# Kernel optimization log

Measured on AMD Instinct MI355X. Metric: run time of the kernel, lower is better.

## Reference

```python
import jax, jax.numpy as jnp
import numpy as np

B, F, D = 2048, 40, 32
CIN = (64, 64)


def _glorot(key, shape):
    fan_in, fan_out = shape[1] * shape[2], shape[0] * shape[2]
    std = jnp.sqrt(2.0 / (fan_in + fan_out)).astype(jnp.float32)
    return jax.random.normal(key, shape, dtype=jnp.float32) * std


def setup_inputs() -> dict:
    key = jax.random.key(0)
    kx, k0, k1 = jax.random.split(key, 3)
    x = jax.random.normal(kx, (B, F, D), dtype=jnp.float32)
    W0 = _glorot(k0, (CIN[0], F * F, D))
    b0 = jnp.zeros((CIN[0],), dtype=jnp.float32)
    W1 = _glorot(k1, (CIN[1], F * CIN[0], D))
    b1 = jnp.zeros((CIN[1],), dtype=jnp.float32)
    return {"x": x, "W0": W0, "b0": b0, "W1": W1, "b1": b1}


def _cin_step(x0, xk, W, b):
    # x0: (B,F,D)  xk: (B,H,D)  W: (O, H*F, D)  b: (O,)
    Bn, H, Dn = xk.shape
    Fn = x0.shape[1]
    # outer product per embedding channel, h-major flatten as in tf.reshape
    z = jnp.einsum('bhd,bfd->bhfd', xk, x0).reshape(Bn, H * Fn, Dn)
    # per-embedding-channel contraction against weights: (B,D,O)
    y = jnp.einsum('bhd,ohd->bdo', z, W) + b
    y = jax.nn.relu(y)
    return jnp.transpose(y, (0, 2, 1))  # (B,O,D)


def reference(x, W0, b0, W1, b1):
    x1 = _cin_step(x, x, W0, b0)
    x2 = _cin_step(x, x1, W1, b1)
    final = jnp.concatenate([x, x1, x2], axis=1)  # (B, F+O0+O1, D)
    return jnp.sum(final, axis=-1)  # (B, F+O0+O1)
```

## Files before the change

### kernel.cpp

```cpp
#include <hip/hip_runtime.h>

typedef unsigned int   u32;
typedef unsigned short u16;
typedef _Float16       f16;

using f16x8  = __attribute__((ext_vector_type(8)))  _Float16;
using f32x16 = __attribute__((ext_vector_type(16))) float;

#define LLDS16(G, L) __builtin_amdgcn_global_load_lds( \
  (const __attribute__((address_space(1))) u32*)(G), \
  (__attribute__((address_space(3))) u32*)(L), 16, 0, 0)

#define WAITV(N) { asm volatile("s_waitcnt vmcnt(" #N ")" ::: "memory"); \
                   __builtin_amdgcn_sched_barrier(0); }
#define FENCE_BAR() { asm volatile("s_waitcnt lgkmcnt(0)" ::: "memory"); \
                      __builtin_amdgcn_sched_barrier(0); \
                      __builtin_amdgcn_s_barrier(); \
                      __builtin_amdgcn_sched_barrier(0); }
#define BAR() { __builtin_amdgcn_s_barrier(); __builtin_amdgcn_sched_barrier(0); }
#define KEEP(x) asm volatile("" : "+v"(x))

__global__ __launch_bounds__(256)
void xprep(const float* __restrict__ in, f16* __restrict__ out,
           float* __restrict__ osum){
  __shared__ float tile[32][33];
  const int tid = threadIdx.x;
  const int r0  = blockIdx.x << 5;
  const int c   = tid & 31;
  const int rp  = tid >> 5;
#pragma unroll
  for (int p = 0; p < 4; ++p){
    const int r = (p << 3) + rp;
    float v = in[(size_t)(r0 + r) * 32 + c];
    tile[r][c] = v;
    float s = v;
#pragma unroll
    for (int off = 16; off > 0; off >>= 1) s += __shfl_xor(s, off, 32);
    if (c == 0){
      const int row = r0 + r;
      osum[(size_t)(row / 40) * 168 + (row % 40)] = s;
    }
  }
  __syncthreads();
#pragma unroll
  for (int p = 0; p < 4; ++p){
    const int dd = (p << 3) + rp;
    out[(size_t)dd * 81920 + r0 + c] = (f16)tile[c][dd];
  }
}

__global__ __launch_bounds__(256)
void wprep(const float* __restrict__ W0, const float* __restrict__ W1,
           f16* __restrict__ out0, f16* __restrict__ out1){
  __shared__ u16 t[32 * 530];
  int kb = blockIdx.x;
  const float* in; f16* out; int K;
  if (kb < 200){ in = W0; out = out0; K = 1600; }
  else         { kb -= 200; in = W1; out = out1; K = 2560; }
  const int tid = threadIdx.x;
  const int kbase = kb << 3;
#pragma unroll 4
  for (int i = 0; i < 64; ++i){
    const int idx = tid + (i << 8);
    const int o   = idx >> 8;
    const int rem = idx & 255;
    const int e   = rem >> 5;
    const int dd  = rem & 31;
    const float v = in[(size_t)o * (K * 32) + (size_t)(kbase + e) * 32 + dd];
    union { f16 h; u16 u; } cv; cv.h = (f16)v;
    t[dd * 530 + o * 8 + e] = cv.u;
  }
  __syncthreads();
  const u32* t32 = (const u32*)t;
  u32* o32 = (u32*)out;
  const int obase = kb << 8;
#pragma unroll 4
  for (int i = 0; i < 32; ++i){
    const int idx = tid + (i << 8);
    const int dd  = idx >> 8;
    const int rem = idx & 255;
    o32[(size_t)dd * (K * 32) + obase + rem] = t32[dd * 265 + rem];
  }
}

template<int H>
__global__ __launch_bounds__(512, 2)
void cin_gemm(const f16* __restrict__ xt,
              const f16* __restrict__ xkt,
              const f16* __restrict__ Wp,
              const float* __restrict__ bias,
              f16*       __restrict__ yt)
{
  constexpr int K     = H * 40;
  constexpr int NT    = K / 320;
  constexpr int X0OFF = 81920;
  constexpr int XKOFF = 110592;
  constexpr int X0MS  = 32 * 112;
  constexpr int XHMS  = (H == 64) ? 32 * 144 : 32 * 112;
  constexpr int SMEM  = (H == 64) ? 147456 : 110592;

  const int bid = blockIdx.x;
  const int d   = ((bid & 7) << 2) | ((bid >> 3) & 3);
  const int b0  = (bid >> 5) << 8;
  const int tid = threadIdx.x;
  const int wv  = tid >> 6;
  const int wr  = wv >> 1;
  const int wc  = wv & 1;
  const int l   = tid & 63;
  const int hi  = l >> 5;
  const int lr  = l & 31;

  __shared__ char smem[SMEM];

  const f16* gW = Wp + (size_t)d * (K * 64);

#define ISSUE_TILE(T, BUF) do { \
    const f16* gt = gW + (size_t)(T) * 20480 + wv * 2560 + l * 8; \
    char* lb = smem + (BUF) * 40960 + wv * 5120; \
    _Pragma("unroll") \
    for (int i = 0; i < 5; ++i) LLDS16(gt + i * 512, lb + i * 1024); \
  } while (0)

  ISSUE_TILE(0, 0);
  ISSUE_TILE(1, 1);

  {
    const uint4* src = (const uint4*)(xt + (size_t)d * 81920 + (size_t)b0 * 40);
#pragma unroll
    for (int it = 0; it < 3; ++it){
      const int idx = tid + (it << 9);
      if (idx < 1280){
        const int r = idx / 5, c = idx - r * 5;
        *(uint4*)(smem + X0OFF + r * 112 + c * 16) = src[idx];
      }
    }
  }
  if constexpr (H == 64){
    const uint4* src = (const uint4*)(xkt + (size_t)d * 131072 + (size_t)b0 * 64);
#pragma unroll
    for (int it = 0; it < 4; ++it){
      const int idx = tid + (it << 9);
      const int r = idx >> 3, c = idx & 7;
      *(uint4*)(smem + XKOFF + r * 144 + c * 16) = src[idx];
    }
  }
  __syncthreads();

  const char* x0row = smem + X0OFF + (wr * 64 + lr) * 112;
  const char* xhrow = (H == 64) ? (smem + XKOFF + (wr * 64 + lr) * 144) : x0row;

  f16x8 sl[2][5];
#pragma unroll
  for (int m = 0; m < 2; ++m){
    const char* xe = x0row + m * X0MS + hi * 16;
#pragma unroll
    for (int t = 0; t < 4; ++t) sl[m][t] = *(const f16x8*)(xe + t * 16);
    sl[m][4] = *(const f16x8*)(x0row + m * X0MS + (hi ? 0 : 64));
  }
  KEEP(sl[0][0]); KEEP(sl[0][1]); KEEP(sl[0][2]); KEEP(sl[0][3]); KEEP(sl[0][4]);
  KEEP(sl[1][0]); KEEP(sl[1][1]); KEEP(sl[1][2]); KEEP(sl[1][3]); KEEP(sl[1][4]);

  f16x8 xh0 = *(const f16x8*)(xhrow);
  f16x8 xh1 = *(const f16x8*)(xhrow + XHMS);

  f32x16 acc0 = {0,0,0,0,0,0,0,0,0,0,0,0,0,0,0,0};
  f32x16 acc1 = {0,0,0,0,0,0,0,0,0,0,0,0,0,0,0,0};

  const int vb = hi * 1024 + wc * 512 + lr * 16;

  static constexpr int J0[10]  = {0,4,3,2,1,0,4,3,2,1};
  static constexpr int H0[10]  = {0,0,1,2,3,4,4,5,6,7};
  static constexpr int H0b[10] = {0,1,1,2,3,4,5,5,6,7};
  static constexpr int S0[10]  = {0,1,0,0,0,0,1,0,0,0};
  static constexpr int J2[10]  = {2,1,0,4,3,2,1,0,4,3};
  static constexpr int H2[10]  = {0,1,2,2,3,4,5,6,6,7};
  static constexpr int H2b[10] = {0,1,2,3,3,4,5,6,7,7};
  static constexpr int S2[10]  = {0,0,0,1,0,0,0,0,1,0};

  for (int t = 0; t < NT; ++t){
    const char* bb = smem + (t & 1) * 40960 + vb;
    const f16x8 xhn0 = *(const f16x8*)(xhrow + (t + 1) * 16);
    const f16x8 xhn1 = *(const f16x8*)(xhrow + XHMS + (t + 1) * 16);
#pragma unroll
    for (int si = 0; si < 10; ++si){
      const f16x8 bf0 = *(const f16x8*)(bb + (si * 4) * 1024);
      const f16x8 bf2 = *(const f16x8*)(bb + (si * 4 + 2) * 1024);
      const f16 xa00 = (S0[si] && hi) ? xh0[H0b[si]] : xh0[H0[si]];
      const f16 xa01 = (S0[si] && hi) ? xh1[H0b[si]] : xh1[H0[si]];
      const f16 xa20 = (S2[si] && hi) ? xh0[H2b[si]] : xh0[H2[si]];
      const f16 xa21 = (S2[si] && hi) ? xh1[H2b[si]] : xh1[H2[si]];
      acc0 = __builtin_amdgcn_mfma_f32_32x32x16_f16(sl[0][J0[si]] * xa00, bf0, acc0, 0, 0, 0);
      acc1 = __builtin_amdgcn_mfma_f32_32x32x16_f16(sl[1][J0[si]] * xa01, bf0, acc1, 0, 0, 0);
      acc0 = __builtin_amdgcn_mfma_f32_32x32x16_f16(sl[0][J2[si]] * xa20, bf2, acc0, 0, 0, 0);
      acc1 = __builtin_amdgcn_mfma_f32_32x32x16_f16(sl[1][J2[si]] * xa21, bf2, acc1, 0, 0, 0);
    }
    FENCE_BAR();
    if (t + 2 < NT){
      ISSUE_TILE(t + 2, t & 1);
      WAITV(5);
    } else {
      WAITV(0);
    }
    BAR();
    xh0 = xhn0; xh1 = xhn1;
  }

  const float bv = bias[(wc << 5) + lr];
  u16* yw = (u16*)(smem + wv * 4608);
#pragma unroll
  for (int m = 0; m < 2; ++m)
#pragma unroll
    for (int reg = 0; reg < 16; ++reg){
      const int row = (m << 5) + (reg & 3) + ((reg >> 2) << 3) + (hi << 2);
      float v = (m ? acc1[reg] : acc0[reg]) + bv;
      v = v > 0.f ? v : 0.f;
      union { f16 h; u16 u; } cv; cv.h = (f16)v;
      yw[row * 36 + lr] = cv.u;
    }
  asm volatile("s_waitcnt lgkmcnt(0)" ::: "memory");
  {
    f16* ydst = yt + (size_t)d * 131072;
#pragma unroll
    for (int j = 0; j < 4; ++j){
      const int row = (j << 4) + (l >> 2);
      const int ch  = l & 3;
      const f16x8 vv = *(const f16x8*)((const char*)yw + row * 72 + ch * 16);
      *(f16x8*)(ydst + (size_t)(b0 + (wr << 6) + row) * 64 + (wc << 5) + (ch << 3)) = vv;
    }
  }
#undef ISSUE_TILE
}

__global__ __launch_bounds__(128)
void finalize(const f16* __restrict__ x1t, const f16* __restrict__ y2t,
              float* __restrict__ out){
  const int b = blockIdx.x;
  const int t = threadIdx.x;
  if (t < 64){
    float s = 0.f;
#pragma unroll
    for (int d = 0; d < 32; ++d) s += (float)x1t[(size_t)d * 131072 + (size_t)b * 64 + t];
    out[(size_t)b * 168 + 40 + t] = s;
  } else {
    const int o = t - 64;
    float s = 0.f;
#pragma unroll
    for (int d = 0; d < 32; ++d) s += (float)y2t[(size_t)d * 131072 + (size_t)b * 64 + o];
    out[(size_t)b * 168 + 104 + o] = s;
  }
}

extern "C" void kernel_launch(void* const* d_in, const int* in_sizes, int n_in,
                              void* d_out, int out_size, void* d_ws, size_t ws_size,
                              hipStream_t stream){
  const float* x   = (const float*)d_in[0];
  const float* W0  = (const float*)d_in[1];
  const float* b0v = (const float*)d_in[2];
  const float* W1  = (const float*)d_in[3];
  const float* b1v = (const float*)d_in[4];
  float* out = (float*)d_out;

  char* ws = (char*)d_ws;
  f16* xt  = (f16*)(ws + 0);
  f16* W0p = (f16*)(ws + 5242880);
  f16* W1p = (f16*)(ws + 11796480);
  f16* x1t = (f16*)(ws + 22282240);
  f16* y2t = (f16*)(ws + 30670848);

  xprep<<<2560, 256, 0, stream>>>(x, xt, out);
  wprep<<<520, 256, 0, stream>>>(W0, W1, W0p, W1p);

  cin_gemm<40><<<256, 512, 0, stream>>>(xt, nullptr, W0p, b0v, x1t);
  cin_gemm<64><<<256, 512, 0, stream>>>(xt, x1t,     W1p, b1v, y2t);

  finalize<<<2048, 128, 0, stream>>>(x1t, y2t, out);
}
```

Before: 62.75 us.

## Fuse both CIN layers into one kernel with atomic row-sum epilogue

```diff
diff --git a/kernel.cpp b/kernel.cpp
--- a/kernel.cpp
+++ b/kernel.cpp
@@ -21,83 +21,78 @@
 #define KEEP(x) asm volatile("" : "+v"(x))
 
 __global__ __launch_bounds__(256)
-void xprep(const float* __restrict__ in, f16* __restrict__ out,
-           float* __restrict__ osum){
-  __shared__ float tile[32][33];
+void prep(const float* __restrict__ x,
+          const float* __restrict__ W0, const float* __restrict__ W1,
+          f16* __restrict__ xt, f16* __restrict__ W0p, f16* __restrict__ W1p,
+          float* __restrict__ out){
+  __shared__ char shm[33920];
   const int tid = threadIdx.x;
-  const int r0  = blockIdx.x << 5;
-  const int c   = tid & 31;
-  const int rp  = tid >> 5;
-#pragma unroll
-  for (int p = 0; p < 4; ++p){
-    const int r = (p << 3) + rp;
-    float v = in[(size_t)(r0 + r) * 32 + c];
-    tile[r][c] = v;
-    float s = v;
-#pragma unroll
-    for (int off = 16; off > 0; off >>= 1) s += __shfl_xor(s, off, 32);
-    if (c == 0){
-      const int row = r0 + r;
-      osum[(size_t)(row / 40) * 168 + (row % 40)] = s;
-    }
-  }
-  __syncthreads();
-#pragma unroll
-  for (int p = 0; p < 4; ++p){
-    const int dd = (p << 3) + rp;
-    out[(size_t)dd * 81920 + r0 + c] = (f16)tile[c][dd];
+  if (blockIdx.x < 2560){
+    float (*tile)[33] = (float(*)[33])shm;
+    const int r0 = blockIdx.x << 5;
+    const int c  = tid & 31;
+    const int rp = tid >> 5;
+#pragma unroll
+    for (int p = 0; p < 4; ++p){
+      const int r = (p << 3) + rp;
+      float v = x[(size_t)(r0 + r) * 32 + c];
+      tile[r][c] = v;
+      float s = v;
+#pragma unroll
+      for (int off = 16; off > 0; off >>= 1) s += __shfl_xor(s, off, 32);
+      if (c == 0){
+        const int row = r0 + r;
+        out[(size_t)(row / 40) * 168 + (row % 40)] = s;
+      }
+    }
+    __syncthreads();
+#pragma unroll
+    for (int p = 0; p < 4; ++p){
+      const int dd = (p << 3) + rp;
+      xt[(size_t)dd * 81920 + r0 + c] = (f16)tile[c][dd];
+    }
+  } else {
+    u16* t = (u16*)shm;
+    int kb = blockIdx.x - 2560;
+    const float* in; f16* outp; int K;
+    if (kb < 200){ in = W0; outp = W0p; K = 1600; }
+    else         { kb -= 200; in = W1; outp = W1p; K = 2560; }
+    const int kbase = kb << 3;
+#pragma unroll 4
+    for (int i = 0; i < 64; ++i){
+      const int idx = tid + (i << 8);
+      const int o   = idx >> 8;
+      const int rem = idx & 255;
+      const int e   = rem >> 5;
+      const int dd  = rem & 31;
+      const float v = in[(size_t)o * (K * 32) + (size_t)(kbase + e) * 32 + dd];
+      union { f16 h; u16 u; } cv; cv.h = (f16)v;
+      t[dd * 530 + o * 8 + e] = cv.u;
+    }
+    __syncthreads();
+    const u32* t32 = (const u32*)t;
+    u32* o32 = (u32*)outp;
+    const int obase = kb << 8;
+#pragma unroll 4
+    for (int i = 0; i < 32; ++i){
+      const int idx = tid + (i << 8);
+      const int dd  = idx >> 8;
+      const int rem = idx & 255;
+      o32[(size_t)dd * (K * 32) + obase + rem] = t32[dd * 265 + rem];
+    }
   }
 }
 
-__global__ __launch_bounds__(256)
-void wprep(const float* __restrict__ W0, const float* __restrict__ W1,
-           f16* __restrict__ out0, f16* __restrict__ out1){
-  __shared__ u16 t[32 * 530];
-  int kb = blockIdx.x;
-  const float* in; f16* out; int K;
-  if (kb < 200){ in = W0; out = out0; K = 1600; }
-  else         { kb -= 200; in = W1; out = out1; K = 2560; }
-  const int tid = threadIdx.x;
-  const int kbase = kb << 3;
-#pragma unroll 4
-  for (int i = 0; i < 64; ++i){
-    const int idx = tid + (i << 8);
-    const int o   = idx >> 8;
-    const int rem = idx & 255;
-    const int e   = rem >> 5;
-    const int dd  = rem & 31;
-    const float v = in[(size_t)o * (K * 32) + (size_t)(kbase + e) * 32 + dd];
-    union { f16 h; u16 u; } cv; cv.h = (f16)v;
-    t[dd * 530 + o * 8 + e] = cv.u;
-  }
-  __syncthreads();
-  const u32* t32 = (const u32*)t;
-  u32* o32 = (u32*)out;
-  const int obase = kb << 8;
-#pragma unroll 4
-  for (int i = 0; i < 32; ++i){
-    const int idx = tid + (i << 8);
-    const int dd  = idx >> 8;
-    const int rem = idx & 255;
-    o32[(size_t)dd * (K * 32) + obase + rem] = t32[dd * 265 + rem];
-  }
-}
-
-template<int H>
-__global__ __launch_bounds__(512, 2)
-void cin_gemm(const f16* __restrict__ xt,
-              const f16* __restrict__ xkt,
-              const f16* __restrict__ Wp,
-              const float* __restrict__ bias,
-              f16*       __restrict__ yt)
-{
-  constexpr int K     = H * 40;
-  constexpr int NT    = K / 320;
+__global__ __launch_bounds__(512, 1)
+void cin_fused(const f16* __restrict__ xt,
+               const f16* __restrict__ W0p,
+               const f16* __restrict__ W1p,
+               const float* __restrict__ b0v, const float* __restrict__ b1v,
+               float* __restrict__ out){
   constexpr int X0OFF = 81920;
-  constexpr int XKOFF = 110592;
+  constexpr int X1OFF = 110592;
   constexpr int X0MS  = 32 * 112;
-  constexpr int XHMS  = (H == 64) ? 32 * 144 : 32 * 112;
-  constexpr int SMEM  = (H == 64) ? 147456 : 110592;
+  constexpr int X1MS  = 32 * 144;
 
   const int bid = blockIdx.x;
   const int d   = ((bid & 7) << 2) | ((bid >> 3) & 3);
@@ -110,19 +105,22 @@
   const int hi  = l >> 5;
   const int lr  = l & 31;
 
-  __shared__ char smem[SMEM];
-
-  const f16* gW = Wp + (size_t)d * (K * 64);
-
-#define ISSUE_TILE(T, BUF) do { \
-    const f16* gt = gW + (size_t)(T) * 20480 + wv * 2560 + l * 8; \
-    char* lb = smem + (BUF) * 40960 + wv * 5120; \
+  __shared__ char smem[147456];
+
+  const f16* gW0 = W0p + (size_t)d * 102400;
+  const f16* gW1 = W1p + (size_t)d * 163840;
+
+#define ISSUE(I) do { \
+    const f16* src_ = ((I) < 5) ? (gW0 + (size_t)(I) * 20480) \
+                                : (gW1 + (size_t)((I) - 5) * 20480); \
+    const f16* gt_ = src_ + wv * 2560 + l * 8; \
+    char* lb_ = smem + ((I) & 1) * 40960 + wv * 5120; \
     _Pragma("unroll") \
-    for (int i = 0; i < 5; ++i) LLDS16(gt + i * 512, lb + i * 1024); \
+    for (int j_ = 0; j_ < 5; ++j_) LLDS16(gt_ + j_ * 512, lb_ + j_ * 1024); \
   } while (0)
 
-  ISSUE_TILE(0, 0);
-  ISSUE_TILE(1, 1);
+  ISSUE(0);
+  ISSUE(1);
 
   {
     const uint4* src = (const uint4*)(xt + (size_t)d * 81920 + (size_t)b0 * 40);
@@ -135,19 +133,13 @@
       }
     }
   }
-  if constexpr (H == 64){
-    const uint4* src = (const uint4*)(xkt + (size_t)d * 131072 + (size_t)b0 * 64);
-#pragma unroll
-    for (int it = 0; it < 4; ++it){
-      const int idx = tid + (it << 9);
-      const int r = idx >> 3, c = idx & 7;
-      *(uint4*)(smem + XKOFF + r * 144 + c * 16) = src[idx];
-    }
-  }
   __syncthreads();
 
   const char* x0row = smem + X0OFF + (wr * 64 + lr) * 112;
-  const char* xhrow = (H == 64) ? (smem + XKOFF + (wr * 64 + lr) * 144) : x0row;
+  const char* x1row = smem + X1OFF + (wr * 64 + lr) * 144;
+  const int   hcol  = (wc << 5) + lr;
+  const float bv1   = b0v[hcol];
+  const float bv2   = b1v[hcol];
 
   f16x8 sl[2][5];
 #pragma unroll
@@ -159,9 +151,6 @@
   }
   KEEP(sl[0][0]); KEEP(sl[0][1]); KEEP(sl[0][2]); KEEP(sl[0][3]); KEEP(sl[0][4]);
   KEEP(sl[1][0]); KEEP(sl[1][1]); KEEP(sl[1][2]); KEEP(sl[1][3]); KEEP(sl[1][4]);
-
-  f16x8 xh0 = *(const f16x8*)(xhrow);
-  f16x8 xh1 = *(const f16x8*)(xhrow + XHMS);
 
   f32x16 acc0 = {0,0,0,0,0,0,0,0,0,0,0,0,0,0,0,0};
   f32x16 acc1 = {0,0,0,0,0,0,0,0,0,0,0,0,0,0,0,0};
@@ -177,77 +166,90 @@
   static constexpr int H2b[10] = {0,1,2,3,3,4,5,6,7,7};
   static constexpr int S2[10]  = {0,0,0,1,0,0,0,0,1,0};
 
-  for (int t = 0; t < NT; ++t){
-    const char* bb = smem + (t & 1) * 40960 + vb;
-    const f16x8 xhn0 = *(const f16x8*)(xhrow + (t + 1) * 16);
-    const f16x8 xhn1 = *(const f16x8*)(xhrow + XHMS + (t + 1) * 16);
-#pragma unroll
-    for (int si = 0; si < 10; ++si){
-      const f16x8 bf0 = *(const f16x8*)(bb + (si * 4) * 1024);
-      const f16x8 bf2 = *(const f16x8*)(bb + (si * 4 + 2) * 1024);
-      const f16 xa00 = (S0[si] && hi) ? xh0[H0b[si]] : xh0[H0[si]];
-      const f16 xa01 = (S0[si] && hi) ? xh1[H0b[si]] : xh1[H0[si]];
-      const f16 xa20 = (S2[si] && hi) ? xh0[H2b[si]] : xh0[H2[si]];
-      const f16 xa21 = (S2[si] && hi) ? xh1[H2b[si]] : xh1[H2[si]];
-      acc0 = __builtin_amdgcn_mfma_f32_32x32x16_f16(sl[0][J0[si]] * xa00, bf0, acc0, 0, 0, 0);
-      acc1 = __builtin_amdgcn_mfma_f32_32x32x16_f16(sl[1][J0[si]] * xa01, bf0, acc1, 0, 0, 0);
-      acc0 = __builtin_amdgcn_mfma_f32_32x32x16_f16(sl[0][J2[si]] * xa20, bf2, acc0, 0, 0, 0);
-      acc1 = __builtin_amdgcn_mfma_f32_32x32x16_f16(sl[1][J2[si]] * xa21, bf2, acc1, 0, 0, 0);
-    }
-    FENCE_BAR();
-    if (t + 2 < NT){
-      ISSUE_TILE(t + 2, t & 1);
+#define COMP(BB) do { \
+  _Pragma("unroll") \
+  for (int si = 0; si < 10; ++si){ \
+    const f16x8 bf0 = *(const f16x8*)((BB) + (si * 4) * 1024); \
+    const f16x8 bf2 = *(const f16x8*)((BB) + (si * 4 + 2) * 1024); \
+    const f16 xa00 = (S0[si] && hi) ? xh0[H0b[si]] : xh0[H0[si]]; \
+    const f16 xa01 = (S0[si] && hi) ? xh1[H0b[si]] : xh1[H0[si]]; \
+    const f16 xa20 = (S2[si] && hi) ? xh0[H2b[si]] : xh0[H2[si]]; \
+    const f16 xa21 = (S2[si] && hi) ? xh1[H2b[si]] : xh1[H2[si]]; \
+    acc0 = __builtin_amdgcn_mfma_f32_32x32x16_f16(sl[0][J0[si]] * xa00, bf0, acc0, 0, 0, 0); \
+    acc1 = __builtin_amdgcn_mfma_f32_32x32x16_f16(sl[1][J0[si]] * xa01, bf0, acc1, 0, 0, 0); \
+    acc0 = __builtin_amdgcn_mfma_f32_32x32x16_f16(sl[0][J2[si]] * xa20, bf2, acc0, 0, 0, 0); \
+    acc1 = __builtin_amdgcn_mfma_f32_32x32x16_f16(sl[1][J2[si]] * xa21, bf2, acc1, 0, 0, 0); \
+  } \
+} while (0)
+
+  {
+    f16x8 xh0 = *(const f16x8*)(x0row);
+    f16x8 xh1 = *(const f16x8*)(x0row + X0MS);
+    for (int t = 0; t < 5; ++t){
+      const char* bb = smem + (t & 1) * 40960 + vb;
+      const f16x8 xhn0 = *(const f16x8*)(x0row + (t + 1) * 16);
+      const f16x8 xhn1 = *(const f16x8*)(x0row + X0MS + (t + 1) * 16);
+      COMP(bb);
+      FENCE_BAR();
+      ISSUE(t + 2);
       WAITV(5);
-    } else {
-      WAITV(0);
-    }
+      BAR();
+      xh0 = xhn0; xh1 = xhn1;
+    }
+  }
+
+  {
+    u16* x1w = (u16*)(smem + X1OFF);
+#pragma unroll
+    for (int m = 0; m < 2; ++m)
+#pragma unroll
+      for (int reg = 0; reg < 16; ++reg){
+        const int row = (wr << 6) + (m << 5) + (reg & 3) + ((reg >> 2) << 3) + (hi << 2);
+        float v = (m ? acc1[reg] : acc0[reg]) + bv1;
+        v = v > 0.f ? v : 0.f;
+        union { f16 h; u16 u; } cv; cv.h = (f16)v;
+        x1w[row * 72 + hcol] = cv.u;
+        atomicAdd(&out[(size_t)(b0 + row) * 168 + 40 + hcol], v);
+      }
+    const f32x16 fz = {0,0,0,0,0,0,0,0,0,0,0,0,0,0,0,0};
+    acc0 = fz; acc1 = fz;
+    asm volatile("s_waitcnt lgkmcnt(0)" ::: "memory");
+    __builtin_amdgcn_sched_barrier(0);
+    WAITV(0);
     BAR();
-    xh0 = xhn0; xh1 = xhn1;
-  }
-
-  const float bv = bias[(wc << 5) + lr];
-  u16* yw = (u16*)(smem + wv * 4608);
+  }
+
+  {
+    f16x8 xh0 = *(const f16x8*)(x1row);
+    f16x8 xh1 = *(const f16x8*)(x1row + X1MS);
+    for (int t = 0; t < 8; ++t){
+      const char* bb = smem + ((t + 1) & 1) * 40960 + vb;
+      const f16x8 xhn0 = *(const f16x8*)(x1row + (t + 1) * 16);
+      const f16x8 xhn1 = *(const f16x8*)(x1row + X1MS + (t + 1) * 16);
+      COMP(bb);
+      FENCE_BAR();
+      if (t + 2 < 8){
+        ISSUE(5 + t + 2);
+        WAITV(5);
+      } else {
+        WAITV(0);
+      }
+      BAR();
+      xh0 = xhn0; xh1 = xhn1;
+    }
+  }
+
 #pragma unroll
   for (int m = 0; m < 2; ++m)
 #pragma unroll
     for (int reg = 0; reg < 16; ++reg){
-      const int row = (m << 5) + (reg & 3) + ((reg >> 2) << 3) + (hi << 2);
-      float v = (m ? acc1[reg] : acc0[reg]) + bv;
+      const int row = (wr << 6) + (m << 5) + (reg & 3) + ((reg >> 2) << 3) + (hi << 2);
+      float v = (m ? acc1[reg] : acc0[reg]) + bv2;
       v = v > 0.f ? v : 0.f;
-      union { f16 h; u16 u; } cv; cv.h = (f16)v;
-      yw[row * 36 + lr] = cv.u;
-    }
-  asm volatile("s_waitcnt lgkmcnt(0)" ::: "memory");
-  {
-    f16* ydst = yt + (size_t)d * 131072;
-#pragma unroll
-    for (int j = 0; j < 4; ++j){
-      const int row = (j << 4) + (l >> 2);
-      const int ch  = l & 3;
-      const f16x8 vv = *(const f16x8*)((const char*)yw + row * 72 + ch * 16);
-      *(f16x8*)(ydst + (size_t)(b0 + (wr << 6) + row) * 64 + (wc << 5) + (ch << 3)) = vv;
-    }
-  }
-#undef ISSUE_TILE
-}
-
-__global__ __launch_bounds__(128)
-void finalize(const f16* __restrict__ x1t, const f16* __restrict__ y2t,
-              float* __restrict__ out){
-  const int b = blockIdx.x;
-  const int t = threadIdx.x;
-  if (t < 64){
-    float s = 0.f;
-#pragma unroll
-    for (int d = 0; d < 32; ++d) s += (float)x1t[(size_t)d * 131072 + (size_t)b * 64 + t];
-    out[(size_t)b * 168 + 40 + t] = s;
-  } else {
-    const int o = t - 64;
-    float s = 0.f;
-#pragma unroll
-    for (int d = 0; d < 32; ++d) s += (float)y2t[(size_t)d * 131072 + (size_t)b * 64 + o];
-    out[(size_t)b * 168 + 104 + o] = s;
-  }
+      atomicAdd(&out[(size_t)(b0 + row) * 168 + 104 + hcol], v);
+    }
+#undef ISSUE
+#undef COMP
 }
 
 extern "C" void kernel_launch(void* const* d_in, const int* in_sizes, int n_in,
@@ -264,14 +266,8 @@
   f16* xt  = (f16*)(ws + 0);
   f16* W0p = (f16*)(ws + 5242880);
   f16* W1p = (f16*)(ws + 11796480);
-  f16* x1t = (f16*)(ws + 22282240);
-  f16* y2t = (f16*)(ws + 30670848);
-
-  xprep<<<2560, 256, 0, stream>>>(x, xt, out);
-  wprep<<<520, 256, 0, stream>>>(W0, W1, W0p, W1p);
-
-  cin_gemm<40><<<256, 512, 0, stream>>>(xt, nullptr, W0p, b0v, x1t);
-  cin_gemm<64><<<256, 512, 0, stream>>>(xt, x1t,     W1p, b1v, y2t);
-
-  finalize<<<2048, 128, 0, stream>>>(x1t, y2t, out);
+
+  hipMemsetAsync(out, 0, (size_t)2048 * 168 * sizeof(float), stream);
+  prep<<<3080, 256, 0, stream>>>(x, W0, W1, xt, W0p, W1p, out);
+  cin_fused<<<256, 512, 0, stream>>>(xt, W0p, W1p, b0v, b1v, out);
 }
```

New measurement: 84.80 us. +35.2%, slower.
